# Optimization experiments

Measured on AMD Instinct MI355X. Metric: run time of the kernel, lower is better.

Reference implementation:

```python
import jax, jax.numpy as jnp
import numpy as np

B, S, D, H, O = 256, 64, 256, 1024, 512
N_CELLS = 3


def setup_inputs() -> dict:
    key = jax.random.key(0)
    ks = jax.random.split(key, 16)

    def u(k, shape, fan):
        return (jax.random.uniform(k, shape, jnp.float32, -1.0, 1.0) / np.float32(np.sqrt(fan)))

    inp = {"inputs": jax.random.normal(ks[0], (B, S, D), jnp.float32)}
    in_dims = [D, H, H]
    i = 1
    for c in range(N_CELLS):
        inp[f"w_ih_{c}"] = u(ks[i], (3 * H, in_dims[c]), H); i += 1
        inp[f"w_hh_{c}"] = u(ks[i], (3 * H, H), H); i += 1
        inp[f"b_ih_{c}"] = u(ks[i], (3 * H,), H); i += 1
        inp[f"b_hh_{c}"] = u(ks[i], (3 * H,), H); i += 1
    inp["lin_w"] = u(ks[13], (S, H, O), H)   # per-step linear weights (same_linear=False)
    inp["lin_b"] = u(ks[14], (S, O), H)
    return inp


def _gru_cell(x, h, w_ih, w_hh, b_ih, b_hh):
    # PyTorch GRUCell gate order: r, z, n
    gi = x @ w_ih.T + b_ih          # [B, 3H]
    gh = h @ w_hh.T + b_hh          # [B, 3H]
    i_r, i_z, i_n = jnp.split(gi, 3, axis=-1)
    h_r, h_z, h_n = jnp.split(gh, 3, axis=-1)
    r = jax.nn.sigmoid(i_r + h_r)
    z = jax.nn.sigmoid(i_z + h_z)
    n = jnp.tanh(i_n + r * h_n)
    return (1.0 - z) * n + z * h


def reference(inputs, w_ih_0, w_hh_0, b_ih_0, b_hh_0,
              w_ih_1, w_hh_1, b_ih_1, b_hh_1,
              w_ih_2, w_hh_2, b_ih_2, b_hh_2,
              lin_w, lin_b):
    params = [(w_ih_0, w_hh_0, b_ih_0, b_hh_0),
              (w_ih_1, w_hh_1, b_ih_1, b_hh_1),
              (w_ih_2, w_hh_2, b_ih_2, b_hh_2)]
    batch = inputs.shape[0]
    hdim = w_hh_0.shape[1]

    def step(hs, xs):
        x_t, wL, bL = xs              # [B,D], [H,O], [O]
        new_hs = []
        cur = x_t
        for i, (wi, wh, bi, bh) in enumerate(params):
            h = _gru_cell(cur, hs[i], wi, wh, bi, bh)
            new_hs.append(h)
            cur = h
        out = cur @ wL + bL           # [B,O]
        return tuple(new_hs), out

    h0 = tuple(jnp.zeros((batch, hdim), inputs.dtype) for _ in range(N_CELLS))
    xs = (jnp.swapaxes(inputs, 0, 1), lin_w, lin_b)  # scan over seq dim
    hs, outs = jax.lax.scan(step, h0, xs)            # outs: [S,B,O]
    return (jnp.swapaxes(outs, 0, 1), hs[0], hs[1], hs[2])
```

## Files before the change

### kernel.cpp

```cpp
#include <hip/hip_runtime.h>
#include <hip/hip_bf16.h>
#include <stdint.h>

#define B_ 256
#define S_ 64
#define D_ 256
#define H_ 1024
#define O_ 512
#define G_ 3072
#define BH_ (B_ * H_)

typedef unsigned short u16;
typedef __attribute__((ext_vector_type(8))) short bf16x8;
typedef __attribute__((ext_vector_type(4))) float f32x4;

#define MFMA16(a, b, c) __builtin_amdgcn_mfma_f32_16x16x32_bf16((a), (b), (c), 0, 0, 0)

__device__ __forceinline__ u16 f2b(float f) {
    union { float f; uint32_t u; } v; v.f = f;
    uint32_t u = v.u;
    uint32_t r = (u + 0x7fffu + ((u >> 16) & 1u)) >> 16;
    return (u16)r;
}
__device__ __forceinline__ float b2f(u16 b) {
    union { uint32_t u; float f; } v; v.u = ((uint32_t)b) << 16;
    return v.f;
}

__device__ __forceinline__ void gl_lds16(const u16* g, u16* l) {
    __builtin_amdgcn_global_load_lds(
        (const __attribute__((address_space(1))) unsigned int*)g,
        (__attribute__((address_space(3))) unsigned int*)l, 16, 0, 0);
}


__global__ void k_conv(const float* __restrict__ s, u16* __restrict__ d, int n) {
    int i = blockIdx.x * blockDim.x + threadIdx.x;
    int st = gridDim.x * blockDim.x;
    for (; i < n; i += st) d[i] = f2b(s[i]);
}

__global__ __launch_bounds__(256) void k_twl(const float* __restrict__ w, u16* __restrict__ o) {
    __shared__ float tile[32][33];
    int bid = blockIdx.x;
    int t = bid >> 9;
    int rem = bid & 511;
    int j0 = (rem >> 4) << 5;
    int o0 = (rem & 15) << 5;
    int tx = threadIdx.x & 31, ty = threadIdx.x >> 5;
    const float* base = w + (size_t)t * (H_ * O_);
#pragma unroll
    for (int i = 0; i < 4; ++i) {
        int r = ty + (i << 3);
        tile[r][tx] = base[(size_t)(j0 + r) * O_ + o0 + tx];
    }
    __syncthreads();
    u16* ob = o + (size_t)t * (O_ * H_);
#pragma unroll
    for (int i = 0; i < 4; ++i) {
        int r = ty + (i << 3);
        ob[(size_t)(o0 + r) * H_ + j0 + tx] = f2b(tile[tx][r]);
    }
}


struct PhaseArgs {
    const u16* Xb;
    const u16 *Wi0, *Wh0, *Wi1, *Wh1, *Wi2, *Wh2;
    const float *bi0, *bh0, *bi1, *bh1, *bi2, *bh2;
    u16 *h0b, *h1b, *h2all;
    float *h0f, *h1f, *h2f;
};

__global__ __launch_bounds__(256) void k_phase(PhaseArgs p, int k) {
    int cell = blockIdx.x >> 6;
    int t = k - cell;
    if (t < 0 || t >= S_) return;
    int tile = blockIdx.x & 63;
    int b0 = (tile >> 4) << 6;
    int j0 = (tile & 15) << 6;

    const u16 *A0, *A1, *Wi, *Wh;
    const float *bi, *bh, *A1f;
    u16* hout;
    float* houtf;
    int ld0, K0;
    if (cell == 0) {
        A0 = p.Xb + t * D_; ld0 = S_ * D_; K0 = D_;
        A1 = p.h0b + ((t + 1) & 1) * BH_;
        A1f = p.h0f + ((t + 1) & 1) * BH_;
        hout = p.h0b + (t & 1) * BH_;
        houtf = p.h0f + (t & 1) * BH_;
        Wi = p.Wi0; Wh = p.Wh0; bi = p.bi0; bh = p.bh0;
    } else if (cell == 1) {
        A0 = p.h0b + (t & 1) * BH_; ld0 = H_; K0 = H_;
        A1 = p.h1b + ((t + 1) & 1) * BH_;
        A1f = p.h1f + ((t + 1) & 1) * BH_;
        hout = p.h1b + (t & 1) * BH_;
        houtf = p.h1f + (t & 1) * BH_;
        Wi = p.Wi1; Wh = p.Wh1; bi = p.bi1; bh = p.bh1;
    } else {
        A0 = p.h1b + (t & 1) * BH_; ld0 = H_; K0 = H_;
        A1 = p.h2all + (size_t)t * BH_;
        A1f = p.h2f + ((t + 1) & 1) * BH_;
        hout = p.h2all + (size_t)(t + 1) * BH_;
        houtf = p.h2f + (t & 1) * BH_;
        Wi = p.Wi2; Wh = p.Wh2; bi = p.bi2; bh = p.bh2;
    }

    __shared__ u16 lds[2][4][64 * 32];

    int tid = threadIdx.x;
    int srow = tid >> 2;
    int ssoff = (((tid & 3) ^ (srow & 3)) << 3);

    int wid = tid >> 6, lane = tid & 63;
    int wr = ((wid >> 1) << 5), wc = ((wid & 1) << 5);
    int fr = lane & 15, kc = lane >> 4;

    int aoff[2], boff[2];
#pragma unroll
    for (int m = 0; m < 2; ++m) {
        int rr = wr + 16 * m + fr;
        aoff[m] = rr * 32 + ((kc ^ (rr & 3)) << 3);
    }
#pragma unroll
    for (int n = 0; n < 2; ++n) {
        int cc = wc + 16 * n + fr;
        boff[n] = cc * 32 + ((kc ^ (cc & 3)) << 3);
    }

    f32x4 accR[2][2] = {{{0.f,0.f,0.f,0.f},{0.f,0.f,0.f,0.f}},{{0.f,0.f,0.f,0.f},{0.f,0.f,0.f,0.f}}};
    f32x4 accZ[2][2] = {{{0.f,0.f,0.f,0.f},{0.f,0.f,0.f,0.f}},{{0.f,0.f,0.f,0.f},{0.f,0.f,0.f,0.f}}};
    f32x4 accI[2][2] = {{{0.f,0.f,0.f,0.f},{0.f,0.f,0.f,0.f}},{{0.f,0.f,0.f,0.f},{0.f,0.f,0.f,0.f}}};
    f32x4 accN[2][2] = {{{0.f,0.f,0.f,0.f},{0.f,0.f,0.f,0.f}},{{0.f,0.f,0.f,0.f},{0.f,0.f,0.f,0.f}}};

    const int n0 = K0 >> 5;
    const int nIt = n0 + (H_ >> 5);

    {
        const u16* Ag = A0 + (size_t)(b0 + srow) * ld0 + ssoff;
        const u16* Wg = Wi + (size_t)(j0 + srow) * K0 + ssoff;
        gl_lds16(Ag, &lds[0][0][tid << 3]);
        gl_lds16(Wg, &lds[0][1][tid << 3]);
        gl_lds16(Wg + (size_t)H_ * K0, &lds[0][2][tid << 3]);
        gl_lds16(Wg + (size_t)(2 * H_) * K0, &lds[0][3][tid << 3]);
    }
    __syncthreads();

    for (int it = 0; it < nIt; ++it) {
        int cur = it & 1;
        int nx = it + 1;
        if (nx < nIt) {
            u16* dA = &lds[cur ^ 1][0][tid << 3];
            u16* dR = &lds[cur ^ 1][1][tid << 3];
            u16* dZ = &lds[cur ^ 1][2][tid << 3];
            u16* dN = &lds[cur ^ 1][3][tid << 3];
            if (nx < n0) {
                int kk = nx << 5;
                const u16* Ag = A0 + (size_t)(b0 + srow) * ld0 + kk + ssoff;
                const u16* Wg = Wi + (size_t)(j0 + srow) * K0 + kk + ssoff;
                gl_lds16(Ag, dA);
                gl_lds16(Wg, dR);
                gl_lds16(Wg + (size_t)H_ * K0, dZ);
                gl_lds16(Wg + (size_t)(2 * H_) * K0, dN);
            } else {
                int kk = (nx - n0) << 5;
                const u16* Ag = A1 + (size_t)(b0 + srow) * H_ + kk + ssoff;
                const u16* Wg = Wh + (size_t)(j0 + srow) * H_ + kk + ssoff;
                gl_lds16(Ag, dA);
                gl_lds16(Wg, dR);
                gl_lds16(Wg + (size_t)H_ * H_, dZ);
                gl_lds16(Wg + (size_t)(2 * H_) * H_, dN);
            }
        }
        bf16x8 a0 = *(const bf16x8*)&lds[cur][0][aoff[0]];
        bf16x8 a1 = *(const bf16x8*)&lds[cur][0][aoff[1]];
        bf16x8 r0 = *(const bf16x8*)&lds[cur][1][boff[0]];
        bf16x8 r1 = *(const bf16x8*)&lds[cur][1][boff[1]];
        bf16x8 z0 = *(const bf16x8*)&lds[cur][2][boff[0]];
        bf16x8 z1 = *(const bf16x8*)&lds[cur][2][boff[1]];
        bf16x8 q0 = *(const bf16x8*)&lds[cur][3][boff[0]];
        bf16x8 q1 = *(const bf16x8*)&lds[cur][3][boff[1]];

        accR[0][0] = MFMA16(a0, r0, accR[0][0]);
        accR[0][1] = MFMA16(a0, r1, accR[0][1]);
        accR[1][0] = MFMA16(a1, r0, accR[1][0]);
        accR[1][1] = MFMA16(a1, r1, accR[1][1]);
        accZ[0][0] = MFMA16(a0, z0, accZ[0][0]);
        accZ[0][1] = MFMA16(a0, z1, accZ[0][1]);
        accZ[1][0] = MFMA16(a1, z0, accZ[1][0]);
        accZ[1][1] = MFMA16(a1, z1, accZ[1][1]);
        if (it < n0) {
            accI[0][0] = MFMA16(a0, q0, accI[0][0]);
            accI[0][1] = MFMA16(a0, q1, accI[0][1]);
            accI[1][0] = MFMA16(a1, q0, accI[1][0]);
            accI[1][1] = MFMA16(a1, q1, accI[1][1]);
        } else {
            accN[0][0] = MFMA16(a0, q0, accN[0][0]);
            accN[0][1] = MFMA16(a0, q1, accN[0][1]);
            accN[1][0] = MFMA16(a1, q0, accN[1][0]);
            accN[1][1] = MFMA16(a1, q1, accN[1][1]);
        }
        __syncthreads();
    }

#pragma unroll
    for (int m = 0; m < 2; ++m)
#pragma unroll
        for (int n = 0; n < 2; ++n) {
            int j = j0 + wc + 16 * n + fr;
            float b_r = bi[j] + bh[j];
            float b_z = bi[H_ + j] + bh[H_ + j];
            float b_i = bi[2 * H_ + j];
            float b_h = bh[2 * H_ + j];
#pragma unroll
            for (int i = 0; i < 4; ++i) {
                int brow = b0 + wr + 16 * m + kc * 4 + i;
                float rv = 1.f / (1.f + __expf(-(accR[m][n][i] + b_r)));
                float zv = 1.f / (1.f + __expf(-(accZ[m][n][i] + b_z)));
                float nv = tanhf(accI[m][n][i] + b_i + rv * (accN[m][n][i] + b_h));
                float hp = A1f[(size_t)brow * H_ + j];
                float hn = (1.f - zv) * nv + zv * hp;
                hout[(size_t)brow * H_ + j] = f2b(hn);
                houtf[(size_t)brow * H_ + j] = hn;
            }
        }
}


__global__ __launch_bounds__(256) void k_linear(const u16* __restrict__ h2all,
                                                const u16* __restrict__ wT,
                                                const float* __restrict__ lb,
                                                float* __restrict__ out) {
    int bid = blockIdx.x;
    int t = bid >> 5;
    int tile = bid & 31;
    int b0 = (tile >> 3) << 6;
    int o0 = (tile & 7) << 6;
    const u16* A = h2all + (size_t)(t + 1) * BH_;
    const u16* W = wT + (size_t)t * (O_ * H_);

    __shared__ u16 lds[2][2][64 * 32];
    int tid = threadIdx.x;
    int srow = tid >> 2;
    int ssoff = (((tid & 3) ^ (srow & 3)) << 3);
    int wid = tid >> 6, lane = tid & 63;
    int wr = ((wid >> 1) << 5), wc = ((wid & 1) << 5);
    int fr = lane & 15, kc = lane >> 4;
    int aoff[2], boff[2];
#pragma unroll
    for (int m = 0; m < 2; ++m) {
        int rr = wr + 16 * m + fr;
        aoff[m] = rr * 32 + ((kc ^ (rr & 3)) << 3);
    }
#pragma unroll
    for (int n = 0; n < 2; ++n) {
        int cc = wc + 16 * n + fr;
        boff[n] = cc * 32 + ((kc ^ (cc & 3)) << 3);
    }
    f32x4 acc[2][2] = {{{0.f,0.f,0.f,0.f},{0.f,0.f,0.f,0.f}},{{0.f,0.f,0.f,0.f},{0.f,0.f,0.f,0.f}}};

    gl_lds16(A + (size_t)(b0 + srow) * H_ + ssoff, &lds[0][0][tid << 3]);
    gl_lds16(W + (size_t)(o0 + srow) * H_ + ssoff, &lds[0][1][tid << 3]);
    __syncthreads();
    for (int it = 0; it < 32; ++it) {
        int cur = it & 1;
        if (it + 1 < 32) {
            int kk = (it + 1) << 5;
            gl_lds16(A + (size_t)(b0 + srow) * H_ + kk + ssoff, &lds[cur ^ 1][0][tid << 3]);
            gl_lds16(W + (size_t)(o0 + srow) * H_ + kk + ssoff, &lds[cur ^ 1][1][tid << 3]);
        }
        bf16x8 a0 = *(const bf16x8*)&lds[cur][0][aoff[0]];
        bf16x8 a1 = *(const bf16x8*)&lds[cur][0][aoff[1]];
        bf16x8 w0 = *(const bf16x8*)&lds[cur][1][boff[0]];
        bf16x8 w1 = *(const bf16x8*)&lds[cur][1][boff[1]];
        acc[0][0] = MFMA16(a0, w0, acc[0][0]);
        acc[0][1] = MFMA16(a0, w1, acc[0][1]);
        acc[1][0] = MFMA16(a1, w0, acc[1][0]);
        acc[1][1] = MFMA16(a1, w1, acc[1][1]);
        __syncthreads();
    }
#pragma unroll
    for (int m = 0; m < 2; ++m)
#pragma unroll
        for (int n = 0; n < 2; ++n) {
            int o = o0 + wc + 16 * n + fr;
            float bb = lb[t * O_ + o];
#pragma unroll
            for (int i = 0; i < 4; ++i) {
                int b = b0 + wr + 16 * m + kc * 4 + i;
                out[((size_t)b * S_ + t) * O_ + o] = acc[m][n][i] + bb;
            }
        }
}


__global__ void k_finals(const float* __restrict__ h0f, const float* __restrict__ h1f,
                         const float* __restrict__ h2f, float* __restrict__ out) {
    int i = blockIdx.x * blockDim.x + threadIdx.x;
    int c = i / BH_, r = i - c * BH_;
    const float* s = (c == 0) ? (h0f + BH_) : (c == 1) ? (h1f + BH_) : (h2f + BH_);
    out[(size_t)B_ * S_ * O_ + (size_t)c * BH_ + r] = s[r];
}


extern "C" void kernel_launch(void* const* d_in, const int* in_sizes, int n_in,
                              void* d_out, int out_size, void* d_ws, size_t ws_size,
                              hipStream_t stream) {
    (void)in_sizes; (void)n_in; (void)out_size; (void)ws_size;
    const float* x   = (const float*)d_in[0];
    const float* wi0 = (const float*)d_in[1];
    const float* wh0 = (const float*)d_in[2];
    const float* bi0 = (const float*)d_in[3];
    const float* bh0 = (const float*)d_in[4];
    const float* wi1 = (const float*)d_in[5];
    const float* wh1 = (const float*)d_in[6];
    const float* bi1 = (const float*)d_in[7];
    const float* bh1 = (const float*)d_in[8];
    const float* wi2 = (const float*)d_in[9];
    const float* wh2 = (const float*)d_in[10];
    const float* bi2 = (const float*)d_in[11];
    const float* bh2 = (const float*)d_in[12];
    const float* lw  = (const float*)d_in[13];
    const float* lb  = (const float*)d_in[14];

    char* base = (char*)d_ws;
    size_t off = 0;
    auto alloc = [&](size_t bytes) {
        char* p = base + off;
        off = (off + bytes + 255) & ~(size_t)255;
        return p;
    };
    u16* Xb  = (u16*)alloc((size_t)B_ * S_ * D_ * 2);
    u16* Wi0 = (u16*)alloc((size_t)G_ * D_ * 2);
    u16* Wh0 = (u16*)alloc((size_t)G_ * H_ * 2);
    u16* Wi1 = (u16*)alloc((size_t)G_ * H_ * 2);
    u16* Wh1 = (u16*)alloc((size_t)G_ * H_ * 2);
    u16* Wi2 = (u16*)alloc((size_t)G_ * H_ * 2);
    u16* Wh2 = (u16*)alloc((size_t)G_ * H_ * 2);
    u16* h0b = (u16*)alloc((size_t)2 * BH_ * 2);
    u16* h1b = (u16*)alloc((size_t)2 * BH_ * 2);
    u16* h2a = (u16*)alloc((size_t)(S_ + 1) * BH_ * 2);
    float* h0f = (float*)alloc((size_t)2 * BH_ * 4);
    float* h1f = (float*)alloc((size_t)2 * BH_ * 4);
    float* h2f = (float*)alloc((size_t)2 * BH_ * 4);
    u16* WLt = (u16*)alloc((size_t)S_ * O_ * H_ * 2);

    k_conv<<<2048, 256, 0, stream>>>(x,   Xb,  B_ * S_ * D_);
    k_conv<<<2048, 256, 0, stream>>>(wi0, Wi0, G_ * D_);
    k_conv<<<2048, 256, 0, stream>>>(wh0, Wh0, G_ * H_);
    k_conv<<<2048, 256, 0, stream>>>(wi1, Wi1, G_ * H_);
    k_conv<<<2048, 256, 0, stream>>>(wh1, Wh1, G_ * H_);
    k_conv<<<2048, 256, 0, stream>>>(wi2, Wi2, G_ * H_);
    k_conv<<<2048, 256, 0, stream>>>(wh2, Wh2, G_ * H_);
    k_twl<<<S_ * 512, 256, 0, stream>>>(lw, WLt);
    hipMemsetAsync(h0b, 0, (size_t)2 * BH_ * 2, stream);
    hipMemsetAsync(h1b, 0, (size_t)2 * BH_ * 2, stream);
    hipMemsetAsync(h2a, 0, (size_t)BH_ * 2, stream);
    hipMemsetAsync(h0f, 0, (size_t)2 * BH_ * 4, stream);
    hipMemsetAsync(h1f, 0, (size_t)2 * BH_ * 4, stream);
    hipMemsetAsync(h2f, 0, (size_t)2 * BH_ * 4, stream);

    PhaseArgs pa;
    pa.Xb = Xb;
    pa.Wi0 = Wi0; pa.Wh0 = Wh0; pa.Wi1 = Wi1; pa.Wh1 = Wh1; pa.Wi2 = Wi2; pa.Wh2 = Wh2;
    pa.bi0 = bi0; pa.bh0 = bh0; pa.bi1 = bi1; pa.bh1 = bh1; pa.bi2 = bi2; pa.bh2 = bh2;
    pa.h0b = h0b; pa.h1b = h1b; pa.h2all = h2a;
    pa.h0f = h0f; pa.h1f = h1f; pa.h2f = h2f;

    for (int k = 0; k < S_ + 2; ++k)
        k_phase<<<192, 256, 0, stream>>>(pa, k);

    k_linear<<<S_ * 32, 256, 0, stream>>>(h2a, WLt, lb, (float*)d_out);
    k_finals<<<(3 * BH_) / 256, 256, 0, stream>>>(h0f, h1f, h2f, (float*)d_out);
}
```

Baseline: 2.617 ms.

## Fuse wavefront GRU phases into one cooperative persistent kernel with split-K waves

Replaces the 66 per-phase kernel launches with a single cooperative kernel that loops over wavefront steps and uses grid.sync between them. Blocks grow to 512 threads with a K-tile of 64; two wave groups each take half of every tile and their partial sums are combined through LDS before the gate epilogue. Blocks are assigned so the same j-columns stay on one XCD, which may improve L2 reuse of weights. Also vectorises the fp32-to-bf16 conversion kernel and changes the LDS swizzle in the linear kernel. The trade-off is the cost of grid-wide barriers, an extra LDS reduction per step, and the requirement that all 192 blocks be co-resident.

```diff
diff --git a/kernel.cpp b/kernel.cpp
--- a/kernel.cpp
+++ b/kernel.cpp
@@ -1,6 +1,9 @@
 #include <hip/hip_runtime.h>
 #include <hip/hip_bf16.h>
+#include <hip/hip_cooperative_groups.h>
 #include <stdint.h>
+
+namespace cg = cooperative_groups;
 
 #define B_ 256
 #define S_ 64
@@ -22,10 +25,6 @@
     uint32_t r = (u + 0x7fffu + ((u >> 16) & 1u)) >> 16;
     return (u16)r;
 }
-__device__ __forceinline__ float b2f(u16 b) {
-    union { uint32_t u; float f; } v; v.u = ((uint32_t)b) << 16;
-    return v.f;
-}
 
 __device__ __forceinline__ void gl_lds16(const u16* g, u16* l) {
     __builtin_amdgcn_global_load_lds(
@@ -34,10 +33,15 @@
 }
 
 
-__global__ void k_conv(const float* __restrict__ s, u16* __restrict__ d, int n) {
+__global__ void k_conv(const float* __restrict__ s, u16* __restrict__ d, int n4) {
     int i = blockIdx.x * blockDim.x + threadIdx.x;
     int st = gridDim.x * blockDim.x;
-    for (; i < n; i += st) d[i] = f2b(s[i]);
+    for (; i < n4; i += st) {
+        float4 v = ((const float4*)s)[i];
+        ushort4 o;
+        o.x = f2b(v.x); o.y = f2b(v.y); o.z = f2b(v.z); o.w = f2b(v.w);
+        ((ushort4*)d)[i] = o;
+    }
 }
 
 __global__ __launch_bounds__(256) void k_twl(const float* __restrict__ w, u16* __restrict__ o) {
@@ -64,168 +68,190 @@
 }
 
 
-struct PhaseArgs {
+struct GruArgs {
     const u16* Xb;
     const u16 *Wi0, *Wh0, *Wi1, *Wh1, *Wi2, *Wh2;
     const float *bi0, *bh0, *bi1, *bh1, *bi2, *bh2;
-    u16 *h0b, *h1b, *h2all;
+    u16 *h0b, *h1b, *h2a;
     float *h0f, *h1f, *h2f;
 };
 
-__global__ __launch_bounds__(256) void k_phase(PhaseArgs p, int k) {
-    int cell = blockIdx.x >> 6;
-    int t = k - cell;
-    if (t < 0 || t >= S_) return;
-    int tile = blockIdx.x & 63;
-    int b0 = (tile >> 4) << 6;
-    int j0 = (tile & 15) << 6;
-
-    const u16 *A0, *A1, *Wi, *Wh;
-    const float *bi, *bh, *A1f;
-    u16* hout;
-    float* houtf;
-    int ld0, K0;
-    if (cell == 0) {
-        A0 = p.Xb + t * D_; ld0 = S_ * D_; K0 = D_;
-        A1 = p.h0b + ((t + 1) & 1) * BH_;
-        A1f = p.h0f + ((t + 1) & 1) * BH_;
-        hout = p.h0b + (t & 1) * BH_;
-        houtf = p.h0f + (t & 1) * BH_;
-        Wi = p.Wi0; Wh = p.Wh0; bi = p.bi0; bh = p.bh0;
-    } else if (cell == 1) {
-        A0 = p.h0b + (t & 1) * BH_; ld0 = H_; K0 = H_;
-        A1 = p.h1b + ((t + 1) & 1) * BH_;
-        A1f = p.h1f + ((t + 1) & 1) * BH_;
-        hout = p.h1b + (t & 1) * BH_;
-        houtf = p.h1f + (t & 1) * BH_;
-        Wi = p.Wi1; Wh = p.Wh1; bi = p.bi1; bh = p.bh1;
-    } else {
-        A0 = p.h1b + (t & 1) * BH_; ld0 = H_; K0 = H_;
-        A1 = p.h2all + (size_t)t * BH_;
-        A1f = p.h2f + ((t + 1) & 1) * BH_;
-        hout = p.h2all + (size_t)(t + 1) * BH_;
-        houtf = p.h2f + (t & 1) * BH_;
-        Wi = p.Wi2; Wh = p.Wh2; bi = p.bi2; bh = p.bh2;
-    }
-
-    __shared__ u16 lds[2][4][64 * 32];
+__global__ __launch_bounds__(512, 2) void k_gru(GruArgs p) {
+    int w = blockIdx.x;
+    int xcd = w & 7;
+    int q = w >> 3;
+    int cell = q >> 3;
+    int r = q & 7;
+    int j0 = ((xcd << 1) + (r >> 2)) << 6;
+    int b0 = (r & 3) << 6;
+
+    const u16 *Wi, *Wh;
+    const float *bi, *bh;
+    int K0;
+    if (cell == 0)      { Wi = p.Wi0; Wh = p.Wh0; bi = p.bi0; bh = p.bh0; K0 = D_; }
+    else if (cell == 1) { Wi = p.Wi1; Wh = p.Wh1; bi = p.bi1; bh = p.bh1; K0 = H_; }
+    else                { Wi = p.Wi2; Wh = p.Wh2; bi = p.bi2; bh = p.bh2; K0 = H_; }
+    const int nX = K0 >> 6;
+    const int nSup = nX + (H_ >> 6);
+
+    __shared__ u16 lds[2][4][64 * 64];
 
     int tid = threadIdx.x;
-    int srow = tid >> 2;
-    int ssoff = (((tid & 3) ^ (srow & 3)) << 3);
+    int srow = tid >> 3;
+    int soff = ((tid & 7) ^ (srow & 7)) << 3;
 
     int wid = tid >> 6, lane = tid & 63;
-    int wr = ((wid >> 1) << 5), wc = ((wid & 1) << 5);
+    int g = wid >> 2;
+    int quad = wid & 3;
+    int wr = (quad >> 1) << 5, wc = (quad & 1) << 5;
     int fr = lane & 15, kc = lane >> 4;
 
     int aoff[2], boff[2];
 #pragma unroll
     for (int m = 0; m < 2; ++m) {
-        int rr = wr + 16 * m + fr;
-        aoff[m] = rr * 32 + ((kc ^ (rr & 3)) << 3);
+        int row = wr + 16 * m + fr;
+        aoff[m] = row * 64 + ((((g << 2) + kc) ^ (row & 7)) << 3);
     }
 #pragma unroll
     for (int n = 0; n < 2; ++n) {
-        int cc = wc + 16 * n + fr;
-        boff[n] = cc * 32 + ((kc ^ (cc & 3)) << 3);
-    }
-
-    f32x4 accR[2][2] = {{{0.f,0.f,0.f,0.f},{0.f,0.f,0.f,0.f}},{{0.f,0.f,0.f,0.f},{0.f,0.f,0.f,0.f}}};
-    f32x4 accZ[2][2] = {{{0.f,0.f,0.f,0.f},{0.f,0.f,0.f,0.f}},{{0.f,0.f,0.f,0.f},{0.f,0.f,0.f,0.f}}};
-    f32x4 accI[2][2] = {{{0.f,0.f,0.f,0.f},{0.f,0.f,0.f,0.f}},{{0.f,0.f,0.f,0.f},{0.f,0.f,0.f,0.f}}};
-    f32x4 accN[2][2] = {{{0.f,0.f,0.f,0.f},{0.f,0.f,0.f,0.f}},{{0.f,0.f,0.f,0.f},{0.f,0.f,0.f,0.f}}};
-
-    const int n0 = K0 >> 5;
-    const int nIt = n0 + (H_ >> 5);
-
-    {
-        const u16* Ag = A0 + (size_t)(b0 + srow) * ld0 + ssoff;
-        const u16* Wg = Wi + (size_t)(j0 + srow) * K0 + ssoff;
-        gl_lds16(Ag, &lds[0][0][tid << 3]);
-        gl_lds16(Wg, &lds[0][1][tid << 3]);
-        gl_lds16(Wg + (size_t)H_ * K0, &lds[0][2][tid << 3]);
-        gl_lds16(Wg + (size_t)(2 * H_) * K0, &lds[0][3][tid << 3]);
-    }
-    __syncthreads();
-
-    for (int it = 0; it < nIt; ++it) {
-        int cur = it & 1;
-        int nx = it + 1;
-        if (nx < nIt) {
-            u16* dA = &lds[cur ^ 1][0][tid << 3];
-            u16* dR = &lds[cur ^ 1][1][tid << 3];
-            u16* dZ = &lds[cur ^ 1][2][tid << 3];
-            u16* dN = &lds[cur ^ 1][3][tid << 3];
-            if (nx < n0) {
-                int kk = nx << 5;
-                const u16* Ag = A0 + (size_t)(b0 + srow) * ld0 + kk + ssoff;
-                const u16* Wg = Wi + (size_t)(j0 + srow) * K0 + kk + ssoff;
-                gl_lds16(Ag, dA);
-                gl_lds16(Wg, dR);
-                gl_lds16(Wg + (size_t)H_ * K0, dZ);
-                gl_lds16(Wg + (size_t)(2 * H_) * K0, dN);
+        int col = wc + 16 * n + fr;
+        boff[n] = col * 64 + ((((g << 2) + kc) ^ (col & 7)) << 3);
+    }
+
+    cg::grid_group grid = cg::this_grid();
+
+    for (int k = 0; k < S_ + 2; ++k) {
+        int t = k - cell;
+        if (t >= 0 && t < S_) {
+            const u16* Ax; int ldax;
+            const u16* Ah;
+            const float* Hpf;
+            u16* hob; float* hof;
+            if (cell == 0) {
+                Ax = p.Xb + (size_t)b0 * (S_ * D_) + t * D_; ldax = S_ * D_;
+                Ah  = p.h0b + ((t + 1) & 1) * BH_ + (size_t)b0 * H_;
+                Hpf = p.h0f + ((t + 1) & 1) * BH_;
+                hob = p.h0b + (t & 1) * BH_;
+                hof = p.h0f + (t & 1) * BH_;
+            } else if (cell == 1) {
+                Ax = p.h0b + (t & 1) * BH_ + (size_t)b0 * H_; ldax = H_;
+                Ah  = p.h1b + ((t + 1) & 1) * BH_ + (size_t)b0 * H_;
+                Hpf = p.h1f + ((t + 1) & 1) * BH_;
+                hob = p.h1b + (t & 1) * BH_;
+                hof = p.h1f + (t & 1) * BH_;
             } else {
-                int kk = (nx - n0) << 5;
-                const u16* Ag = A1 + (size_t)(b0 + srow) * H_ + kk + ssoff;
-                const u16* Wg = Wh + (size_t)(j0 + srow) * H_ + kk + ssoff;
-                gl_lds16(Ag, dA);
-                gl_lds16(Wg, dR);
-                gl_lds16(Wg + (size_t)H_ * H_, dZ);
-                gl_lds16(Wg + (size_t)(2 * H_) * H_, dN);
+                Ax = p.h1b + (t & 1) * BH_ + (size_t)b0 * H_; ldax = H_;
+                Ah  = p.h2a + (size_t)t * BH_ + (size_t)b0 * H_;
+                Hpf = p.h2f + ((t + 1) & 1) * BH_;
+                hob = p.h2a + (size_t)(t + 1) * BH_;
+                hof = p.h2f + (t & 1) * BH_;
             }
+
+            auto stage = [&](int s, int nb) {
+                const u16 *arow, *wrow; size_t gs;
+                if (s < nX) {
+                    int kk = s << 6;
+                    arow = Ax + (size_t)srow * ldax + kk + soff;
+                    wrow = Wi + (size_t)(j0 + srow) * K0 + kk + soff;
+                    gs = (size_t)H_ * K0;
+                } else {
+                    int kk = (s - nX) << 6;
+                    arow = Ah + (size_t)srow * H_ + kk + soff;
+                    wrow = Wh + (size_t)(j0 + srow) * H_ + kk + soff;
+                    gs = (size_t)H_ * H_;
+                }
+                gl_lds16(arow,          &lds[nb][0][tid << 3]);
+                gl_lds16(wrow,          &lds[nb][1][tid << 3]);
+                gl_lds16(wrow + gs,     &lds[nb][2][tid << 3]);
+                gl_lds16(wrow + 2 * gs, &lds[nb][3][tid << 3]);
+            };
+
+            f32x4 accR[2][2] = {}, accZ[2][2] = {}, accI[2][2] = {}, accN[2][2] = {};
+
+            stage(0, 0);
+            __syncthreads();
+
+            for (int s = 0; s < nSup; ++s) {
+                int cur = s & 1;
+                if (s + 1 < nSup) stage(s + 1, cur ^ 1);
+
+                bf16x8 a0 = *(const bf16x8*)&lds[cur][0][aoff[0]];
+                bf16x8 a1 = *(const bf16x8*)&lds[cur][0][aoff[1]];
+                bf16x8 r0 = *(const bf16x8*)&lds[cur][1][boff[0]];
+                bf16x8 r1 = *(const bf16x8*)&lds[cur][1][boff[1]];
+                bf16x8 z0 = *(const bf16x8*)&lds[cur][2][boff[0]];
+                bf16x8 z1 = *(const bf16x8*)&lds[cur][2][boff[1]];
+                bf16x8 q0 = *(const bf16x8*)&lds[cur][3][boff[0]];
+                bf16x8 q1 = *(const bf16x8*)&lds[cur][3][boff[1]];
+
+                accR[0][0] = MFMA16(a0, r0, accR[0][0]);
+                accR[0][1] = MFMA16(a0, r1, accR[0][1]);
+                accR[1][0] = MFMA16(a1, r0, accR[1][0]);
+                accR[1][1] = MFMA16(a1, r1, accR[1][1]);
+                accZ[0][0] = MFMA16(a0, z0, accZ[0][0]);
+                accZ[0][1] = MFMA16(a0, z1, accZ[0][1]);
+                accZ[1][0] = MFMA16(a1, z0, accZ[1][0]);
+                accZ[1][1] = MFMA16(a1, z1, accZ[1][1]);
+                if (s < nX) {
+                    accI[0][0] = MFMA16(a0, q0, accI[0][0]);
+                    accI[0][1] = MFMA16(a0, q1, accI[0][1]);
+                    accI[1][0] = MFMA16(a1, q0, accI[1][0]);
+                    accI[1][1] = MFMA16(a1, q1, accI[1][1]);
+                } else {
+                    accN[0][0] = MFMA16(a0, q0, accN[0][0]);
+                    accN[0][1] = MFMA16(a0, q1, accN[0][1]);
+                    accN[1][0] = MFMA16(a1, q0, accN[1][0]);
+                    accN[1][1] = MFMA16(a1, q1, accN[1][1]);
+                }
+                __syncthreads();
+            }
+
+            float* red = (float*)&lds[0][0][0];
+            if (g == 1) {
+#pragma unroll
+                for (int m = 0; m < 2; ++m)
+#pragma unroll
+                    for (int n = 0; n < 2; ++n) {
+                        int mn = (m << 1) | n;
+                        *(f32x4*)&red[((((quad << 2) + 0) << 2 | mn) * 64 + lane) << 2] = accR[m][n];
+                        *(f32x4*)&red[((((quad << 2) + 1) << 2 | mn) * 64 + lane) << 2] = accZ[m][n];
+                        *(f32x4*)&red[((((quad << 2) + 2) << 2 | mn) * 64 + lane) << 2] = accI[m][n];
+                        *(f32x4*)&red[((((quad << 2) + 3) << 2 | mn) * 64 + lane) << 2] = accN[m][n];
+                    }
+            }
+            __syncthreads();
+            if (g == 0) {
+#pragma unroll
+                for (int m = 0; m < 2; ++m)
+#pragma unroll
+                    for (int n = 0; n < 2; ++n) {
+                        int mn = (m << 1) | n;
+                        accR[m][n] += *(const f32x4*)&red[((((quad << 2) + 0) << 2 | mn) * 64 + lane) << 2];
+                        accZ[m][n] += *(const f32x4*)&red[((((quad << 2) + 1) << 2 | mn) * 64 + lane) << 2];
+                        accI[m][n] += *(const f32x4*)&red[((((quad << 2) + 2) << 2 | mn) * 64 + lane) << 2];
+                        accN[m][n] += *(const f32x4*)&red[((((quad << 2) + 3) << 2 | mn) * 64 + lane) << 2];
+                        int j = j0 + wc + 16 * n + fr;
+                        float b_r = bi[j] + bh[j];
+                        float b_z = bi[H_ + j] + bh[H_ + j];
+                        float b_i = bi[2 * H_ + j];
+                        float b_h = bh[2 * H_ + j];
+#pragma unroll
+                        for (int i = 0; i < 4; ++i) {
+                            int brow = b0 + wr + 16 * m + kc * 4 + i;
+                            float rv = 1.f / (1.f + __expf(-(accR[m][n][i] + b_r)));
+                            float zv = 1.f / (1.f + __expf(-(accZ[m][n][i] + b_z)));
+                            float nv = tanhf(accI[m][n][i] + b_i + rv * (accN[m][n][i] + b_h));
+                            float hp = Hpf[(size_t)brow * H_ + j];
+                            float hn = (1.f - zv) * nv + zv * hp;
+                            hob[(size_t)brow * H_ + j] = f2b(hn);
+                            hof[(size_t)brow * H_ + j] = hn;
+                        }
+                    }
+            }
+            __syncthreads();
         }
-        bf16x8 a0 = *(const bf16x8*)&lds[cur][0][aoff[0]];
-        bf16x8 a1 = *(const bf16x8*)&lds[cur][0][aoff[1]];
-        bf16x8 r0 = *(const bf16x8*)&lds[cur][1][boff[0]];
-        bf16x8 r1 = *(const bf16x8*)&lds[cur][1][boff[1]];
-        bf16x8 z0 = *(const bf16x8*)&lds[cur][2][boff[0]];
-        bf16x8 z1 = *(const bf16x8*)&lds[cur][2][boff[1]];
-        bf16x8 q0 = *(const bf16x8*)&lds[cur][3][boff[0]];
-        bf16x8 q1 = *(const bf16x8*)&lds[cur][3][boff[1]];
-
-        accR[0][0] = MFMA16(a0, r0, accR[0][0]);
-        accR[0][1] = MFMA16(a0, r1, accR[0][1]);
-        accR[1][0] = MFMA16(a1, r0, accR[1][0]);
-        accR[1][1] = MFMA16(a1, r1, accR[1][1]);
-        accZ[0][0] = MFMA16(a0, z0, accZ[0][0]);
-        accZ[0][1] = MFMA16(a0, z1, accZ[0][1]);
-        accZ[1][0] = MFMA16(a1, z0, accZ[1][0]);
-        accZ[1][1] = MFMA16(a1, z1, accZ[1][1]);
-        if (it < n0) {
-            accI[0][0] = MFMA16(a0, q0, accI[0][0]);
-            accI[0][1] = MFMA16(a0, q1, accI[0][1]);
-            accI[1][0] = MFMA16(a1, q0, accI[1][0]);
-            accI[1][1] = MFMA16(a1, q1, accI[1][1]);
-        } else {
-            accN[0][0] = MFMA16(a0, q0, accN[0][0]);
-            accN[0][1] = MFMA16(a0, q1, accN[0][1]);
-            accN[1][0] = MFMA16(a1, q0, accN[1][0]);
-            accN[1][1] = MFMA16(a1, q1, accN[1][1]);
-        }
-        __syncthreads();
-    }
-
-#pragma unroll
-    for (int m = 0; m < 2; ++m)
-#pragma unroll
-        for (int n = 0; n < 2; ++n) {
-            int j = j0 + wc + 16 * n + fr;
-            float b_r = bi[j] + bh[j];
-            float b_z = bi[H_ + j] + bh[H_ + j];
-            float b_i = bi[2 * H_ + j];
-            float b_h = bh[2 * H_ + j];
-#pragma unroll
-            for (int i = 0; i < 4; ++i) {
-                int brow = b0 + wr + 16 * m + kc * 4 + i;
-                float rv = 1.f / (1.f + __expf(-(accR[m][n][i] + b_r)));
-                float zv = 1.f / (1.f + __expf(-(accZ[m][n][i] + b_z)));
-                float nv = tanhf(accI[m][n][i] + b_i + rv * (accN[m][n][i] + b_h));
-                float hp = A1f[(size_t)brow * H_ + j];
-                float hn = (1.f - zv) * nv + zv * hp;
-                hout[(size_t)brow * H_ + j] = f2b(hn);
-                houtf[(size_t)brow * H_ + j] = hn;
-            }
-        }
+        grid.sync();
+    }
 }
 
 
@@ -244,7 +270,7 @@
     __shared__ u16 lds[2][2][64 * 32];
     int tid = threadIdx.x;
     int srow = tid >> 2;
-    int ssoff = (((tid & 3) ^ (srow & 3)) << 3);
+    int ssoff = ((tid & 3) ^ ((srow >> 1) & 3)) << 3;
     int wid = tid >> 6, lane = tid & 63;
     int wr = ((wid >> 1) << 5), wc = ((wid & 1) << 5);
     int fr = lane & 15, kc = lane >> 4;
@@ -252,14 +278,14 @@
 #pragma unroll
     for (int m = 0; m < 2; ++m) {
         int rr = wr + 16 * m + fr;
-        aoff[m] = rr * 32 + ((kc ^ (rr & 3)) << 3);
+        aoff[m] = rr * 32 + ((kc ^ ((rr >> 1) & 3)) << 3);
     }
 #pragma unroll
     for (int n = 0; n < 2; ++n) {
         int cc = wc + 16 * n + fr;
-        boff[n] = cc * 32 + ((kc ^ (cc & 3)) << 3);
-    }
-    f32x4 acc[2][2] = {{{0.f,0.f,0.f,0.f},{0.f,0.f,0.f,0.f}},{{0.f,0.f,0.f,0.f},{0.f,0.f,0.f,0.f}}};
+        boff[n] = cc * 32 + ((kc ^ ((cc >> 1) & 3)) << 3);
+    }
+    f32x4 acc[2][2] = {};
 
     gl_lds16(A + (size_t)(b0 + srow) * H_ + ssoff, &lds[0][0][tid << 3]);
     gl_lds16(W + (size_t)(o0 + srow) * H_ + ssoff, &lds[0][1][tid << 3]);
@@ -347,13 +373,13 @@
     float* h2f = (float*)alloc((size_t)2 * BH_ * 4);
     u16* WLt = (u16*)alloc((size_t)S_ * O_ * H_ * 2);
 
-    k_conv<<<2048, 256, 0, stream>>>(x,   Xb,  B_ * S_ * D_);
-    k_conv<<<2048, 256, 0, stream>>>(wi0, Wi0, G_ * D_);
-    k_conv<<<2048, 256, 0, stream>>>(wh0, Wh0, G_ * H_);
-    k_conv<<<2048, 256, 0, stream>>>(wi1, Wi1, G_ * H_);
-    k_conv<<<2048, 256, 0, stream>>>(wh1, Wh1, G_ * H_);
-    k_conv<<<2048, 256, 0, stream>>>(wi2, Wi2, G_ * H_);
-    k_conv<<<2048, 256, 0, stream>>>(wh2, Wh2, G_ * H_);
+    k_conv<<<1024, 256, 0, stream>>>(x,   Xb,  (B_ * S_ * D_) / 4);
+    k_conv<<<1024, 256, 0, stream>>>(wi0, Wi0, (G_ * D_) / 4);
+    k_conv<<<1024, 256, 0, stream>>>(wh0, Wh0, (G_ * H_) / 4);
+    k_conv<<<1024, 256, 0, stream>>>(wi1, Wi1, (G_ * H_) / 4);
+    k_conv<<<1024, 256, 0, stream>>>(wh1, Wh1, (G_ * H_) / 4);
+    k_conv<<<1024, 256, 0, stream>>>(wi2, Wi2, (G_ * H_) / 4);
+    k_conv<<<1024, 256, 0, stream>>>(wh2, Wh2, (G_ * H_) / 4);
     k_twl<<<S_ * 512, 256, 0, stream>>>(lw, WLt);
     hipMemsetAsync(h0b, 0, (size_t)2 * BH_ * 2, stream);
     hipMemsetAsync(h1b, 0, (size_t)2 * BH_ * 2, stream);
@@ -362,15 +388,15 @@
     hipMemsetAsync(h1f, 0, (size_t)2 * BH_ * 4, stream);
     hipMemsetAsync(h2f, 0, (size_t)2 * BH_ * 4, stream);
 
-    PhaseArgs pa;
-    pa.Xb = Xb;
-    pa.Wi0 = Wi0; pa.Wh0 = Wh0; pa.Wi1 = Wi1; pa.Wh1 = Wh1; pa.Wi2 = Wi2; pa.Wh2 = Wh2;
-    pa.bi0 = bi0; pa.bh0 = bh0; pa.bi1 = bi1; pa.bh1 = bh1; pa.bi2 = bi2; pa.bh2 = bh2;
-    pa.h0b = h0b; pa.h1b = h1b; pa.h2all = h2a;
-    pa.h0f = h0f; pa.h1f = h1f; pa.h2f = h2f;
-
-    for (int k = 0; k < S_ + 2; ++k)
-        k_phase<<<192, 256, 0, stream>>>(pa, k);
+    GruArgs ga;
+    ga.Xb = Xb;
+    ga.Wi0 = Wi0; ga.Wh0 = Wh0; ga.Wi1 = Wi1; ga.Wh1 = Wh1; ga.Wi2 = Wi2; ga.Wh2 = Wh2;
+    ga.bi0 = bi0; ga.bh0 = bh0; ga.bi1 = bi1; ga.bh1 = bh1; ga.bi2 = bi2; ga.bh2 = bh2;
+    ga.h0b = h0b; ga.h1b = h1b; ga.h2a = h2a;
+    ga.h0f = h0f; ga.h1f = h1f; ga.h2f = h2f;
+
+    void* args[] = {&ga};
+    hipLaunchCooperativeKernel((void*)k_gru, dim3(192), dim3(512), args, 0, stream);
 
     k_linear<<<S_ * 32, 256, 0, stream>>>(h2a, WLt, lb, (float*)d_out);
     k_finals<<<(3 * BH_) / 256, 256, 0, stream>>>(h0f, h1f, h2f, (float*)d_out);
```

New measurement: 3.350 ms, median of 2. 1.28x slower.
